# Performance work log

Measured on AMD Instinct MI355X. Metric: run time of the kernel, lower is better.

Reference implementation:

```python
import jax, jax.numpy as jnp
import numpy as np

D_MODEL = 1024
N_HEADS = 16
HEAD_DIM = D_MODEL // N_HEADS


def setup_inputs() -> dict:
    key = jax.random.key(0)
    k_x, k_wqkv, k_bqkv, k_wp, k_bp = jax.random.split(key, 5)
    B, S = 4, 2048
    bound_qkv = 1.0 / np.sqrt(D_MODEL)
    bound_p = 1.0 / np.sqrt(D_MODEL)
    return {
        "x": jax.random.normal(k_x, (B, S, D_MODEL), dtype=jnp.float32),
        # torch nn.Linear weight is [out, in]; store transposed [in, out] for x @ W
        "w_qkv": jax.random.uniform(k_wqkv, (D_MODEL, 3 * D_MODEL), minval=-bound_qkv, maxval=bound_qkv, dtype=jnp.float32),
        "b_qkv": jax.random.uniform(k_bqkv, (3 * D_MODEL,), minval=-bound_qkv, maxval=bound_qkv, dtype=jnp.float32),
        "w_proj": jax.random.uniform(k_wp, (D_MODEL, D_MODEL), minval=-bound_p, maxval=bound_p, dtype=jnp.float32),
        "b_proj": jax.random.uniform(k_bp, (D_MODEL,), minval=-bound_p, maxval=bound_p, dtype=jnp.float32),
    }


def reference(x, w_qkv, b_qkv, w_proj, b_proj):
    B, S, C = x.shape
    qkv = x @ w_qkv + b_qkv  # [B, S, 3C]
    q, k, v = jnp.split(qkv, 3, axis=-1)
    # [B, H, S, Dh]
    q = q.reshape(B, S, N_HEADS, HEAD_DIM).transpose(0, 2, 1, 3)
    k = k.reshape(B, S, N_HEADS, HEAD_DIM).transpose(0, 2, 1, 3)
    v = v.reshape(B, S, N_HEADS, HEAD_DIM).transpose(0, 2, 1, 3)
    scale = 1.0 / np.sqrt(HEAD_DIM).astype(np.float32)
    att = jnp.einsum("bhqd,bhkd->bhqk", q, k) * scale  # [B, H, S, S]
    causal = jnp.tril(jnp.ones((S, S), dtype=bool))
    att = jnp.where(causal[None, None], att, -jnp.inf)
    att = jax.nn.softmax(att, axis=-1)
    # dropout p=0.0 -> identity
    y = jnp.einsum("bhqk,bhkd->bhqd", att, v)  # [B, H, S, Dh]
    y = y.transpose(0, 2, 1, 3).reshape(B, S, C)
    return y @ w_proj + b_proj
```

## Files before the change

kernel.cpp:

```cpp
#include <hip/hip_runtime.h>
#include <stdint.h>

typedef __attribute__((ext_vector_type(8))) short bf8_t;
typedef __attribute__((ext_vector_type(4))) short bf4_t;
typedef __attribute__((ext_vector_type(4))) float f4_t;

#define D_MODEL 1024
#define SEQ 2048
#define NB 4
#define NH 16
#define HD 64
#define MROWS (NB * SEQ)
#define QSCALE 0.1803368801111204f

__device__ __forceinline__ uint16_t f2bf(float f) {
  uint32_t u = __builtin_bit_cast(uint32_t, f);
  u += 0x7FFFu + ((u >> 16) & 1u);
  return (uint16_t)(u >> 16);
}

__device__ __forceinline__ void gload16(const void* g, void* l) {
  __builtin_amdgcn_global_load_lds(
      (const __attribute__((address_space(1))) void*)g,
      (__attribute__((address_space(3))) void*)l, 16, 0, 0);
}

__global__ void k_cvt(const float* __restrict__ in, uint16_t* __restrict__ out, int n4) {
  int i = blockIdx.x * blockDim.x + threadIdx.x;
  if (i >= n4) return;
  float4 v = ((const float4*)in)[i];
  ushort4 o;
  o.x = f2bf(v.x); o.y = f2bf(v.y); o.z = f2bf(v.z); o.w = f2bf(v.w);
  ((ushort4*)out)[i] = o;
}

__global__ void k_tcvt(const float* __restrict__ in, uint16_t* __restrict__ out, int K, int N) {
  __shared__ float tile[32][33];
  int nb = blockIdx.x * 32, kb = blockIdx.y * 32;
  int tx = threadIdx.x & 31, ty = threadIdx.x >> 5;
#pragma unroll
  for (int i = 0; i < 4; ++i)
    tile[ty + i * 8][tx] = in[(size_t)(kb + ty + i * 8) * N + nb + tx];
  __syncthreads();
#pragma unroll
  for (int i = 0; i < 4; ++i)
    out[(size_t)(nb + ty + i * 8) * K + kb + tx] = f2bf(tile[tx][ty + i * 8]);
}

__device__ __forceinline__ void gemm_mainloop(const uint16_t* __restrict__ A,
                                              const uint16_t* __restrict__ Bt,
                                              int mBase, int nBase, f4_t acc[4][4],
                                              uint16_t* As, uint16_t* Bs) {
  const int t = threadIdx.x;
  const int lane = t & 63;
  const int wm = (t >> 6) >> 1, wn = (t >> 6) & 1;
  for (int ks = 0; ks < D_MODEL / 64; ++ks) {
#pragma unroll
    for (int iss = 0; iss < 4; ++iss) {
      int p = iss * 256 + t;
      int r = p >> 3;
      int c = (p & 7) ^ (r & 7);
      gload16(A + (size_t)(mBase + r) * D_MODEL + ks * 64 + c * 8, As + p * 8);
      gload16(Bt + (size_t)(nBase + r) * D_MODEL + ks * 64 + c * 8, Bs + p * 8);
    }
    __syncthreads();
    bf8_t af[4][2], bfr[4][2];
#pragma unroll
    for (int mi = 0; mi < 4; ++mi) {
      int r = wm * 64 + mi * 16 + (lane & 15);
#pragma unroll
      for (int kx = 0; kx < 2; ++kx) {
        int gl = (lane >> 4) + kx * 4;
        af[mi][kx] = *(const bf8_t*)((const char*)As + r * 128 + ((gl ^ (r & 7)) * 16));
      }
    }
#pragma unroll
    for (int ni = 0; ni < 4; ++ni) {
      int r = wn * 64 + ni * 16 + (lane & 15);
#pragma unroll
      for (int kx = 0; kx < 2; ++kx) {
        int gl = (lane >> 4) + kx * 4;
        bfr[ni][kx] = *(const bf8_t*)((const char*)Bs + r * 128 + ((gl ^ (r & 7)) * 16));
      }
    }
#pragma unroll
    for (int mi = 0; mi < 4; ++mi)
#pragma unroll
      for (int ni = 0; ni < 4; ++ni) {
        acc[mi][ni] = __builtin_amdgcn_mfma_f32_16x16x32_bf16(af[mi][0], bfr[ni][0], acc[mi][ni], 0, 0, 0);
        acc[mi][ni] = __builtin_amdgcn_mfma_f32_16x16x32_bf16(af[mi][1], bfr[ni][1], acc[mi][ni], 0, 0, 0);
      }
    __syncthreads();
  }
}

__global__ __launch_bounds__(256, 2) void k_gemm_qkv(
    const uint16_t* __restrict__ A, const uint16_t* __restrict__ Bt,
    const float* __restrict__ bias,
    uint16_t* __restrict__ Qb, uint16_t* __restrict__ Kb, uint16_t* __restrict__ VTb) {
  __shared__ uint16_t As[128 * 64];
  __shared__ uint16_t Bs[128 * 64];
  f4_t acc[4][4] = {};
  int mBase = blockIdx.y * 128, nBase = blockIdx.x * 128;
  gemm_mainloop(A, Bt, mBase, nBase, acc, As, Bs);
  const int lane = threadIdx.x & 63;
  const int wm = (threadIdx.x >> 6) >> 1, wn = (threadIdx.x >> 6) & 1;
#pragma unroll
  for (int mi = 0; mi < 4; ++mi)
#pragma unroll
    for (int ni = 0; ni < 4; ++ni)
#pragma unroll
      for (int i = 0; i < 4; ++i) {
        int m = mBase + wm * 64 + mi * 16 + (lane >> 4) * 4 + i;
        int n = nBase + wn * 64 + ni * 16 + (lane & 15);
        float v = acc[mi][ni][i] + bias[n];
        int b = m >> 11, s = m & 2047;
        int which = n >> 10, hn = n & 1023;
        int h = hn >> 6, d = hn & 63;
        size_t bh = (size_t)(b * NH + h);
        if (which == 0)      Qb[(bh * SEQ + s) * HD + d] = f2bf(v * QSCALE);
        else if (which == 1) Kb[(bh * SEQ + s) * HD + d] = f2bf(v);
        else                 VTb[(bh * HD + d) * SEQ + s] = f2bf(v);
      }
}

__global__ __launch_bounds__(256, 2) void k_gemm_proj(
    const uint16_t* __restrict__ A, const uint16_t* __restrict__ Bt,
    const float* __restrict__ bias, float* __restrict__ out) {
  __shared__ uint16_t As[128 * 64];
  __shared__ uint16_t Bs[128 * 64];
  f4_t acc[4][4] = {};
  int mBase = blockIdx.y * 128, nBase = blockIdx.x * 128;
  gemm_mainloop(A, Bt, mBase, nBase, acc, As, Bs);
  const int lane = threadIdx.x & 63;
  const int wm = (threadIdx.x >> 6) >> 1, wn = (threadIdx.x >> 6) & 1;
#pragma unroll
  for (int mi = 0; mi < 4; ++mi)
#pragma unroll
    for (int ni = 0; ni < 4; ++ni)
#pragma unroll
      for (int i = 0; i < 4; ++i) {
        int m = mBase + wm * 64 + mi * 16 + (lane >> 4) * 4 + i;
        int n = nBase + wn * 64 + ni * 16 + (lane & 15);
        out[(size_t)m * D_MODEL + n] = acc[mi][ni][i] + bias[n];
      }
}

__global__ __launch_bounds__(512, 4) void k_attn(
    const uint16_t* __restrict__ Qb, const uint16_t* __restrict__ Kb,
    const uint16_t* __restrict__ VTb, uint16_t* __restrict__ Yb) {
  __shared__ uint16_t Ks[2][64 * 64];
  __shared__ uint16_t Vs[2][64 * 64];
  const int t = threadIdx.x, lane = t & 63, wave = t >> 6;
  const int g = lane >> 4, a = lane & 15;
  const int bh = blockIdx.x, pr = blockIdx.y;
  const int b = bh >> 4, h = bh & 15;

  const int sr = t >> 3;
  const int scol = (t & 7) ^ (sr & 7);
  const uint16_t* Kg = Kb + ((size_t)bh * SEQ + sr) * HD + scol * 8;
  const uint16_t* Vg = VTb + ((size_t)bh * HD + sr) * SEQ + scol * 8;

#pragma unroll 1
  for (int seg = 0; seg < 2; ++seg) {
    const int qt = seg ? (15 - pr) : pr;
    const int qrow0 = qt * 128 + wave * 16;
    const uint16_t* Qrow = Qb + ((size_t)bh * SEQ + qrow0 + a) * HD;
    bf8_t aq[2];
    aq[0] = *(const bf8_t*)(Qrow + g * 8);
    aq[1] = *(const bf8_t*)(Qrow + g * 8 + 32);
    float m_i = -__builtin_inff(), l_i = 0.f;
    f4_t O[4] = {};

    const int nt = 2 * qt + 2;
    gload16(Kg, Ks[0] + t * 8);
    gload16(Vg, Vs[0] + t * 8);

    for (int kt = 0; kt < nt; ++kt) {
      const int cur = kt & 1;
      if (kt + 1 < nt) {
        gload16(Kg + (size_t)(kt + 1) * 64 * HD, Ks[cur ^ 1] + t * 8);
        gload16(Vg + (kt + 1) * 64, Vs[cur ^ 1] + t * 8);
        asm volatile("s_waitcnt vmcnt(2)" ::: "memory");
      } else {
        asm volatile("s_waitcnt vmcnt(0)" ::: "memory");
      }
      __builtin_amdgcn_s_barrier();

      const uint16_t* Kt = Ks[cur];
      const uint16_t* Vt = Vs[cur];
      if (kt * 64 <= qrow0 + 15) {
        f4_t sacc[4] = {};
#pragma unroll
        for (int f = 0; f < 4; ++f) {
          int kr = f * 16 + a;
#pragma unroll
          for (int kx = 0; kx < 2; ++kx) {
            int gl = g + kx * 4;
            bf8_t bk = *(const bf8_t*)((const char*)Kt + kr * 128 + ((gl ^ (kr & 7)) * 16));
            sacc[f] = __builtin_amdgcn_mfma_f32_16x16x32_bf16(bk, aq[kx], sacc[f], 0, 0, 0);
          }
        }
        if (kt >= 2 * qt) {
          int q = qrow0 + a;
#pragma unroll
          for (int f = 0; f < 4; ++f)
#pragma unroll
            for (int i = 0; i < 4; ++i) {
              int key = kt * 64 + f * 16 + g * 4 + i;
              if (key > q) sacc[f][i] = -__builtin_inff();
            }
        }
        float mx = sacc[0][0];
#pragma unroll
        for (int f = 0; f < 4; ++f)
#pragma unroll
          for (int i = 0; i < 4; ++i) mx = fmaxf(mx, sacc[f][i]);
        mx = fmaxf(mx, __shfl_xor(mx, 16));
        mx = fmaxf(mx, __shfl_xor(mx, 32));
        if (__any(mx > m_i + 8.0f)) {
          float mN = fmaxf(m_i, mx);
          float sc2 = exp2f(m_i - mN);
          m_i = mN;
          l_i *= sc2;
#pragma unroll
          for (int i = 0; i < 4; ++i) {
            float s4 = __shfl(sc2, (lane & 48) | (g * 4 + i));
#pragma unroll
            for (int f2 = 0; f2 < 4; ++f2) O[f2][i] *= s4;
          }
        }
        float pvv[4][4];
        float sm = 0.f;
#pragma unroll
        for (int f = 0; f < 4; ++f)
#pragma unroll
          for (int i = 0; i < 4; ++i) {
            pvv[f][i] = exp2f(sacc[f][i] - m_i);
            sm += pvv[f][i];
          }
        sm += __shfl_xor(sm, 16);
        sm += __shfl_xor(sm, 32);
        l_i += sm;
        bf8_t pa[2];
#pragma unroll
        for (int kx = 0; kx < 2; ++kx)
#pragma unroll
          for (int j = 0; j < 8; ++j)
            pa[kx][j] = (short)f2bf(pvv[2 * kx + (j >> 2)][j & 3]);
#pragma unroll
        for (int kx = 0; kx < 2; ++kx)
#pragma unroll
          for (int f2 = 0; f2 < 4; ++f2) {
            int rv = f2 * 16 + a;
            int sw = (rv & 7) << 4;
            bf4_t lo = *(const bf4_t*)((const char*)Vt + rv * 128 + ((64 * kx + 8 * g) ^ sw));
            bf4_t hi = *(const bf4_t*)((const char*)Vt + rv * 128 + ((64 * kx + 32 + 8 * g) ^ sw));
            bf8_t bv = __builtin_shufflevector(lo, hi, 0, 1, 2, 3, 4, 5, 6, 7);
            O[f2] = __builtin_amdgcn_mfma_f32_16x16x32_bf16(pa[kx], bv, O[f2], 0, 0, 0);
          }
      }
      asm volatile("s_waitcnt lgkmcnt(0)" ::: "memory");
      __builtin_amdgcn_s_barrier();
    }
    float rinv[4];
#pragma unroll
    for (int i = 0; i < 4; ++i)
      rinv[i] = 1.0f / __shfl(l_i, (lane & 48) | (g * 4 + i));
#pragma unroll
    for (int f2 = 0; f2 < 4; ++f2)
#pragma unroll
      for (int i = 0; i < 4; ++i) {
        int q = qrow0 + g * 4 + i;
        int d = f2 * 16 + a;
        Yb[((size_t)b * SEQ + q) * D_MODEL + h * HD + d] = f2bf(O[f2][i] * rinv[i]);
      }
  }
}

extern "C" void kernel_launch(void* const* d_in, const int* in_sizes, int n_in,
                              void* d_out, int out_size, void* d_ws, size_t ws_size,
                              hipStream_t stream) {
  const float* x     = (const float*)d_in[0];
  const float* wqkv  = (const float*)d_in[1];
  const float* bqkv  = (const float*)d_in[2];
  const float* wproj = (const float*)d_in[3];
  const float* bproj = (const float*)d_in[4];
  float* out = (float*)d_out;
  char* ws = (char*)d_ws;
  uint16_t* xb     = (uint16_t*)(ws);
  uint16_t* wqkvT  = (uint16_t*)(ws + 16777216);
  uint16_t* wprojT = (uint16_t*)(ws + 16777216 + 6291456);
  uint16_t* Qb     = (uint16_t*)(ws + 25165824);
  uint16_t* Kb     = (uint16_t*)(ws + 25165824 + 16777216);
  uint16_t* VTb    = (uint16_t*)(ws + 25165824 + 2 * 16777216);
  uint16_t* Yb     = (uint16_t*)(ws + 25165824 + 3 * 16777216);

  k_cvt<<<dim3(MROWS * D_MODEL / 4 / 256), dim3(256), 0, stream>>>(x, xb, MROWS * D_MODEL / 4);
  k_tcvt<<<dim3(3 * D_MODEL / 32, D_MODEL / 32), dim3(256), 0, stream>>>(wqkv, wqkvT, D_MODEL, 3 * D_MODEL);
  k_tcvt<<<dim3(D_MODEL / 32, D_MODEL / 32), dim3(256), 0, stream>>>(wproj, wprojT, D_MODEL, D_MODEL);
  k_gemm_qkv<<<dim3(3 * D_MODEL / 128, MROWS / 128), dim3(256), 0, stream>>>(xb, wqkvT, bqkv, Qb, Kb, VTb);
  k_attn<<<dim3(NB * NH, 8), dim3(512), 0, stream>>>(Qb, Kb, VTb, Yb);
  k_gemm_proj<<<dim3(D_MODEL / 128, MROWS / 128), dim3(256), 0, stream>>>(Yb, wprojT, bproj, out);
}
```

Before: 280.1 us.

## Double-buffer GEMM mainloop with larger 256-row tiles and swizzled block order

Rewrites the QKV and projection GEMM mainloops to prefetch the next K-tile into a second LDS buffer while computing the current one, using explicit vmcnt waits and raw barriers. Tiles grow to 256x256 (QKV) and 256x128 (proj) with 512-thread blocks, MFMA sections get raised priority, and blocks are remapped in groups of 8 for L2 locality. Bias is hoisted into registers. This aims to hide global load latency and raise reuse, at the cost of more LDS (128KB for QKV) and registers, which lowers occupancy.

```diff
diff --git a/kernel.cpp b/kernel.cpp
--- a/kernel.cpp
+++ b/kernel.cpp
@@ -47,73 +47,111 @@
     out[(size_t)(nb + ty + i * 8) * K + kb + tx] = f2bf(tile[tx][ty + i * 8]);
 }
 
-__device__ __forceinline__ void gemm_mainloop(const uint16_t* __restrict__ A,
-                                              const uint16_t* __restrict__ Bt,
-                                              int mBase, int nBase, f4_t acc[4][4],
-                                              uint16_t* As, uint16_t* Bs) {
-  const int t = threadIdx.x;
-  const int lane = t & 63;
-  const int wm = (t >> 6) >> 1, wn = (t >> 6) & 1;
-  for (int ks = 0; ks < D_MODEL / 64; ++ks) {
-#pragma unroll
-    for (int iss = 0; iss < 4; ++iss) {
-      int p = iss * 256 + t;
-      int r = p >> 3;
-      int c = (p & 7) ^ (r & 7);
-      gload16(A + (size_t)(mBase + r) * D_MODEL + ks * 64 + c * 8, As + p * 8);
-      gload16(Bt + (size_t)(nBase + r) * D_MODEL + ks * 64 + c * 8, Bs + p * 8);
+template <int MREP, int NWN, int BROWS>
+__device__ __forceinline__ void mainloop8(const uint16_t* __restrict__ A,
+                                          const uint16_t* __restrict__ Bt,
+                                          int mBase, int nBase,
+                                          uint16_t* __restrict__ AsB,
+                                          uint16_t* __restrict__ BsB,
+                                          f4_t (&acc)[MREP][4]) {
+  constexpr int BLOADS = BROWS / 64;
+  const int t = threadIdx.x, lane = t & 63;
+  const int g = lane >> 4, a = lane & 15;
+  const int wave = t >> 6, wm = wave / NWN, wn = wave % NWN;
+  const int sr = t >> 3;
+  const int sc = (t & 7) ^ (sr & 7);
+  const uint16_t* Ag[4];
+  const uint16_t* Bg[BLOADS];
+#pragma unroll
+  for (int l = 0; l < 4; ++l)
+    Ag[l] = A + (size_t)(mBase + l * 64 + sr) * D_MODEL + sc * 8;
+#pragma unroll
+  for (int l = 0; l < BLOADS; ++l)
+    Bg[l] = Bt + (size_t)(nBase + l * 64 + sr) * D_MODEL + sc * 8;
+
+  auto stage = [&](int kt, int buf) {
+#pragma unroll
+    for (int l = 0; l < 4; ++l)
+      gload16(Ag[l] + kt * 64, AsB + buf * (256 * 64) + (l * 512 + t) * 8);
+#pragma unroll
+    for (int l = 0; l < BLOADS; ++l)
+      gload16(Bg[l] + kt * 64, BsB + buf * (BROWS * 64) + (l * 512 + t) * 8);
+  };
+
+  stage(0, 0);
+  for (int kt = 0; kt < D_MODEL / 64; ++kt) {
+    const int buf = kt & 1;
+    if (kt < D_MODEL / 64 - 1) {
+      stage(kt + 1, buf ^ 1);
+      if constexpr (BLOADS == 4) asm volatile("s_waitcnt vmcnt(8)" ::: "memory");
+      else                       asm volatile("s_waitcnt vmcnt(6)" ::: "memory");
+    } else {
+      asm volatile("s_waitcnt vmcnt(0)" ::: "memory");
     }
-    __syncthreads();
-    bf8_t af[4][2], bfr[4][2];
-#pragma unroll
-    for (int mi = 0; mi < 4; ++mi) {
-      int r = wm * 64 + mi * 16 + (lane & 15);
-#pragma unroll
-      for (int kx = 0; kx < 2; ++kx) {
-        int gl = (lane >> 4) + kx * 4;
-        af[mi][kx] = *(const bf8_t*)((const char*)As + r * 128 + ((gl ^ (r & 7)) * 16));
-      }
+    __builtin_amdgcn_s_barrier();
+    __builtin_amdgcn_sched_barrier(0);
+    const char* Ab = (const char*)(AsB + buf * (256 * 64));
+    const char* Bb = (const char*)(BsB + buf * (BROWS * 64));
+    bf8_t bfr[4][2];
+#pragma unroll
+    for (int ni = 0; ni < 4; ++ni) {
+      int row = wn * 64 + ni * 16 + a;
+#pragma unroll
+      for (int kk = 0; kk < 2; ++kk)
+        bfr[ni][kk] = *(const bf8_t*)(Bb + row * 128 + (((4 * kk + g) ^ (row & 7)) * 16));
     }
 #pragma unroll
-    for (int ni = 0; ni < 4; ++ni) {
-      int r = wn * 64 + ni * 16 + (lane & 15);
-#pragma unroll
-      for (int kx = 0; kx < 2; ++kx) {
-        int gl = (lane >> 4) + kx * 4;
-        bfr[ni][kx] = *(const bf8_t*)((const char*)Bs + r * 128 + ((gl ^ (r & 7)) * 16));
-      }
+    for (int s = 0; s < MREP / 2; ++s) {
+      bf8_t af[2][2];
+#pragma unroll
+      for (int mm = 0; mm < 2; ++mm) {
+        int row = wm * (MREP * 16) + (2 * s + mm) * 16 + a;
+#pragma unroll
+        for (int kk = 0; kk < 2; ++kk)
+          af[mm][kk] = *(const bf8_t*)(Ab + row * 128 + (((4 * kk + g) ^ (row & 7)) * 16));
+      }
+      __builtin_amdgcn_s_setprio(1);
+#pragma unroll
+      for (int mm = 0; mm < 2; ++mm)
+#pragma unroll
+        for (int ni = 0; ni < 4; ++ni) {
+          acc[2 * s + mm][ni] = __builtin_amdgcn_mfma_f32_16x16x32_bf16(af[mm][0], bfr[ni][0], acc[2 * s + mm][ni], 0, 0, 0);
+          acc[2 * s + mm][ni] = __builtin_amdgcn_mfma_f32_16x16x32_bf16(af[mm][1], bfr[ni][1], acc[2 * s + mm][ni], 0, 0, 0);
+        }
+      __builtin_amdgcn_s_setprio(0);
     }
-#pragma unroll
-    for (int mi = 0; mi < 4; ++mi)
-#pragma unroll
-      for (int ni = 0; ni < 4; ++ni) {
-        acc[mi][ni] = __builtin_amdgcn_mfma_f32_16x16x32_bf16(af[mi][0], bfr[ni][0], acc[mi][ni], 0, 0, 0);
-        acc[mi][ni] = __builtin_amdgcn_mfma_f32_16x16x32_bf16(af[mi][1], bfr[ni][1], acc[mi][ni], 0, 0, 0);
-      }
-    __syncthreads();
+    asm volatile("s_waitcnt lgkmcnt(0)" ::: "memory");
+    __builtin_amdgcn_s_barrier();
+    __builtin_amdgcn_sched_barrier(0);
   }
 }
 
-__global__ __launch_bounds__(256, 2) void k_gemm_qkv(
+__global__ __launch_bounds__(512, 2) void k_gemm_qkv(
     const uint16_t* __restrict__ A, const uint16_t* __restrict__ Bt,
     const float* __restrict__ bias,
     uint16_t* __restrict__ Qb, uint16_t* __restrict__ Kb, uint16_t* __restrict__ VTb) {
-  __shared__ uint16_t As[128 * 64];
-  __shared__ uint16_t Bs[128 * 64];
-  f4_t acc[4][4] = {};
-  int mBase = blockIdx.y * 128, nBase = blockIdx.x * 128;
-  gemm_mainloop(A, Bt, mBase, nBase, acc, As, Bs);
-  const int lane = threadIdx.x & 63;
-  const int wm = (threadIdx.x >> 6) >> 1, wn = (threadIdx.x >> 6) & 1;
-#pragma unroll
-  for (int mi = 0; mi < 4; ++mi)
+  __shared__ uint16_t As[2][256 * 64];
+  __shared__ uint16_t Bs[2][256 * 64];
+  int flat = blockIdx.x;
+  int swz = (flat & 7) * 48 + (flat >> 3);
+  int bx = swz % 12, by = swz / 12;
+  int mBase = by * 256, nBase = bx * 256;
+  f4_t acc[8][4] = {};
+  mainloop8<8, 4, 256>(A, Bt, mBase, nBase, &As[0][0], &Bs[0][0], acc);
+  const int lane = threadIdx.x & 63, g = lane >> 4, a = lane & 15;
+  const int wave = threadIdx.x >> 6, wm = wave >> 2, wn = wave & 3;
+  float bi[4];
+#pragma unroll
+  for (int ni = 0; ni < 4; ++ni) bi[ni] = bias[nBase + wn * 64 + ni * 16 + a];
+#pragma unroll
+  for (int mi = 0; mi < 8; ++mi)
 #pragma unroll
     for (int ni = 0; ni < 4; ++ni)
 #pragma unroll
       for (int i = 0; i < 4; ++i) {
-        int m = mBase + wm * 64 + mi * 16 + (lane >> 4) * 4 + i;
-        int n = nBase + wn * 64 + ni * 16 + (lane & 15);
-        float v = acc[mi][ni][i] + bias[n];
+        int m = mBase + wm * 128 + mi * 16 + 4 * g + i;
+        int n = nBase + wn * 64 + ni * 16 + a;
+        float v = acc[mi][ni][i] + bi[ni];
         int b = m >> 11, s = m & 2047;
         int which = n >> 10, hn = n & 1023;
         int h = hn >> 6, d = hn & 63;
@@ -124,25 +162,31 @@
       }
 }
 
-__global__ __launch_bounds__(256, 2) void k_gemm_proj(
+__global__ __launch_bounds__(512, 2) void k_gemm_proj(
     const uint16_t* __restrict__ A, const uint16_t* __restrict__ Bt,
     const float* __restrict__ bias, float* __restrict__ out) {
-  __shared__ uint16_t As[128 * 64];
-  __shared__ uint16_t Bs[128 * 64];
+  __shared__ uint16_t As[2][256 * 64];
+  __shared__ uint16_t Bs[2][128 * 64];
+  int flat = blockIdx.x;
+  int swz = (flat & 7) * 32 + (flat >> 3);
+  int bx = swz % 8, by = swz / 8;
+  int mBase = by * 256, nBase = bx * 128;
   f4_t acc[4][4] = {};
-  int mBase = blockIdx.y * 128, nBase = blockIdx.x * 128;
-  gemm_mainloop(A, Bt, mBase, nBase, acc, As, Bs);
-  const int lane = threadIdx.x & 63;
-  const int wm = (threadIdx.x >> 6) >> 1, wn = (threadIdx.x >> 6) & 1;
+  mainloop8<4, 2, 128>(A, Bt, mBase, nBase, &As[0][0], &Bs[0][0], acc);
+  const int lane = threadIdx.x & 63, g = lane >> 4, a = lane & 15;
+  const int wave = threadIdx.x >> 6, wm = wave >> 1, wn = wave & 1;
+  float bi[4];
+#pragma unroll
+  for (int ni = 0; ni < 4; ++ni) bi[ni] = bias[nBase + wn * 64 + ni * 16 + a];
 #pragma unroll
   for (int mi = 0; mi < 4; ++mi)
 #pragma unroll
     for (int ni = 0; ni < 4; ++ni)
 #pragma unroll
       for (int i = 0; i < 4; ++i) {
-        int m = mBase + wm * 64 + mi * 16 + (lane >> 4) * 4 + i;
-        int n = nBase + wn * 64 + ni * 16 + (lane & 15);
-        out[(size_t)m * D_MODEL + n] = acc[mi][ni][i] + bias[n];
+        int m = mBase + wm * 64 + mi * 16 + 4 * g + i;
+        int n = nBase + wn * 64 + ni * 16 + a;
+        out[(size_t)m * D_MODEL + n] = acc[mi][ni][i] + bi[ni];
       }
 }
 
@@ -299,7 +343,7 @@
   k_cvt<<<dim3(MROWS * D_MODEL / 4 / 256), dim3(256), 0, stream>>>(x, xb, MROWS * D_MODEL / 4);
   k_tcvt<<<dim3(3 * D_MODEL / 32, D_MODEL / 32), dim3(256), 0, stream>>>(wqkv, wqkvT, D_MODEL, 3 * D_MODEL);
   k_tcvt<<<dim3(D_MODEL / 32, D_MODEL / 32), dim3(256), 0, stream>>>(wproj, wprojT, D_MODEL, D_MODEL);
-  k_gemm_qkv<<<dim3(3 * D_MODEL / 128, MROWS / 128), dim3(256), 0, stream>>>(xb, wqkvT, bqkv, Qb, Kb, VTb);
+  k_gemm_qkv<<<dim3(384), dim3(512), 0, stream>>>(xb, wqkvT, bqkv, Qb, Kb, VTb);
   k_attn<<<dim3(NB * NH, 8), dim3(512), 0, stream>>>(Qb, Kb, VTb, Yb);
-  k_gemm_proj<<<dim3(D_MODEL / 128, MROWS / 128), dim3(256), 0, stream>>>(Yb, wprojT, bproj, out);
-}
+  k_gemm_proj<<<dim3(256), dim3(512), 0, stream>>>(Yb, wprojT, bproj, out);
+}
```

After: 303.8 us. 8.5% more time.
